# Performance work log

Hardware: AMD Instinct MI355X
Metric: run time of the kernel (lower is better)

Reference implementation:

```python
import jax, jax.numpy as jnp
import numpy as np

N_NODES = 50000
N_EDGES = 1600000
HIDDEN = 128
SPATIAL = 3
SCORE_HIDDEN = 128
EPS = 1e-12


def setup_inputs() -> dict:
    key = jax.random.key(0)
    ks = jax.random.split(key, 12)
    s = 0.02
    return {
        "h": jax.random.normal(ks[0], (N_NODES, HIDDEN), dtype=jnp.float32),
        "edge_index": jax.random.randint(ks[1], (2, N_EDGES), 0, N_NODES, dtype=jnp.int64),
        "rel_pos": jax.random.normal(ks[2], (N_EDGES, SPATIAL), dtype=jnp.float32),
        "distance": jax.random.uniform(ks[3], (N_EDGES, 1), dtype=jnp.float32),
        "node_weight": jax.random.uniform(ks[4], (N_NODES,), dtype=jnp.float32),
        "W1": jax.random.normal(ks[5], (2 * HIDDEN + SPATIAL + 1, SCORE_HIDDEN), dtype=jnp.float32) * s,
        "b1": jnp.zeros((SCORE_HIDDEN,), dtype=jnp.float32),
        "W2": jax.random.normal(ks[6], (SCORE_HIDDEN, SCORE_HIDDEN), dtype=jnp.float32) * s,
        "b2": jnp.zeros((SCORE_HIDDEN,), dtype=jnp.float32),
        "W3": jax.random.normal(ks[7], (SCORE_HIDDEN, 1), dtype=jnp.float32) * s,
        "b3": jnp.zeros((1,), dtype=jnp.float32),
        "Wv": jax.random.normal(ks[8], (HIDDEN, HIDDEN), dtype=jnp.float32) * s,
    }


def reference(h, edge_index, rel_pos, distance, node_weight, W1, b1, W2, b2, W3, b3, Wv):
    num_nodes = h.shape[0]
    dst, src = edge_index[0], edge_index[1]
    # per-edge gathered feature: [E, 2*H + spatial + 1]
    edge_feat = jnp.concatenate([h[dst], h[src], rel_pos, distance], axis=-1)
    # 3-layer score MLP -> scalar score per edge
    x = jax.nn.silu(edge_feat @ W1 + b1)
    x = jax.nn.silu(x @ W2 + b2)
    scores = (x @ W3 + b3)[:, 0]  # [E]
    # edge softmax over incoming edges of each dst node
    mx = jax.ops.segment_max(scores, dst, num_segments=num_nodes)  # -inf for empty segments
    exp_scores = jnp.exp(scores - mx[dst])
    den = jax.ops.segment_sum(exp_scores, dst, num_segments=num_nodes)
    alpha = exp_scores / (den[dst] + EPS)
    # value projection, weighted message, scatter-add aggregation
    msg = (h[src] @ Wv) * (alpha * node_weight[src])[:, None]
    out = jax.ops.segment_sum(msg, dst, num_segments=num_nodes)
    return h + out
```

## Files before the change

### kernel.cpp

```cpp
#include <hip/hip_runtime.h>
#include <hip/hip_bf16.h>
#include <cstdint>
#include <cstddef>

#define N_NODES 50000
#define N_EDGES 1600000
#define HID 128
#define PCAT_N 384
#define EPSV 1e-12f

typedef __bf16 bf16_t;
typedef __bf16 bf16x8 __attribute__((ext_vector_type(8)));
typedef float f32x4 __attribute__((ext_vector_type(4)));

__device__ __forceinline__ float bf2f_lo(unsigned u) {
    return __builtin_bit_cast(float, u << 16);
}
__device__ __forceinline__ float bf2f_hi(unsigned u) {
    return __builtin_bit_cast(float, u & 0xFFFF0000u);
}
__device__ __forceinline__ unsigned short f2bf_rne(float x) {
    unsigned u = __builtin_bit_cast(unsigned, x);
    u += 0x7FFFu + ((u >> 16) & 1u);
    return (unsigned short)(u >> 16);
}
__device__ __forceinline__ float silu_f(float x) {
    return x * __builtin_amdgcn_rcpf(1.0f + __expf(-x));
}

__global__ void k_prepw(const float* __restrict__ W1, const float* __restrict__ W2,
                        const float* __restrict__ Wv, bf16_t* __restrict__ wcatT,
                        bf16_t* __restrict__ w2t) {
    int idx = blockIdx.x * blockDim.x + threadIdx.x;
    if (idx < 384 * 128) {
        int n = idx >> 7, k = idx & 127;
        float v;
        if (n < 128)      v = W1[k * 128 + n];
        else if (n < 256) v = W1[(128 + k) * 128 + (n - 128)];
        else              v = Wv[k * 128 + (n - 256)];
        wcatT[idx] = __builtin_bit_cast(bf16_t, f2bf_rne(v));
    } else if (idx < 384 * 128 + 128 * 128) {
        int j = idx - 384 * 128;
        int n = j >> 7, k = j & 127;
        w2t[j] = __builtin_bit_cast(bf16_t, f2bf_rne(W2[k * 128 + n]));
    }
}

__global__ __launch_bounds__(256) void k_nodeproj(
    const float* __restrict__ h, const bf16_t* __restrict__ wcatT,
    const float* __restrict__ nw, bf16_t* __restrict__ pcat) {
    __shared__ bf16_t As[64 * 136];
    int t = threadIdx.x;
    int r0 = blockIdx.x * 64;
    {
        int r = t >> 2, cbase = (t & 3) * 32;
        int gr = r0 + r;
        if (gr >= N_NODES) gr = 0;
        const float* src = h + (size_t)gr * 128 + cbase;
        bf16_t* dst = As + r * 136 + cbase;
#pragma unroll
        for (int i = 0; i < 4; ++i) {
            float4 v0 = *reinterpret_cast<const float4*>(src + i * 8);
            float4 v1 = *reinterpret_cast<const float4*>(src + i * 8 + 4);
            uint4 pk;
            pk.x = (unsigned)f2bf_rne(v0.x) | ((unsigned)f2bf_rne(v0.y) << 16);
            pk.y = (unsigned)f2bf_rne(v0.z) | ((unsigned)f2bf_rne(v0.w) << 16);
            pk.z = (unsigned)f2bf_rne(v1.x) | ((unsigned)f2bf_rne(v1.y) << 16);
            pk.w = (unsigned)f2bf_rne(v1.z) | ((unsigned)f2bf_rne(v1.w) << 16);
            *reinterpret_cast<uint4*>(dst + i * 8) = pk;
        }
    }
    __syncthreads();
    int lane = t & 63, w = t >> 6;
    f32x4 acc[4][6] = {};
#pragma unroll
    for (int kk = 0; kk < 4; ++kk) {
        bf16x8 af[4], bfr[6];
#pragma unroll
        for (int fm = 0; fm < 4; ++fm)
            af[fm] = *reinterpret_cast<const bf16x8*>(
                As + (fm * 16 + (lane & 15)) * 136 + kk * 32 + (lane >> 4) * 8);
#pragma unroll
        for (int fn = 0; fn < 6; ++fn) {
            int n = w * 96 + fn * 16 + (lane & 15);
            bfr[fn] = *reinterpret_cast<const bf16x8*>(
                wcatT + (size_t)n * 128 + kk * 32 + (lane >> 4) * 8);
        }
#pragma unroll
        for (int fm = 0; fm < 4; ++fm)
#pragma unroll
            for (int fn = 0; fn < 6; ++fn)
                acc[fm][fn] = __builtin_amdgcn_mfma_f32_16x16x32_bf16(
                    af[fm], bfr[fn], acc[fm][fn], 0, 0, 0);
    }
#pragma unroll
    for (int fm = 0; fm < 4; ++fm) {
#pragma unroll
        for (int j = 0; j < 4; ++j) {
            int row = r0 + fm * 16 + (lane >> 4) * 4 + j;
            if (row < N_NODES) {
                float nwv = (w >= 2) ? nw[row] : 1.0f;
#pragma unroll
                for (int fn = 0; fn < 6; ++fn) {
                    int colbase = w * 96 + fn * 16;
                    float v = acc[fm][fn][j];
                    if (colbase >= 256) v *= nwv;
                    pcat[(size_t)row * PCAT_N + colbase + (lane & 15)] =
                        __builtin_bit_cast(bf16_t, f2bf_rne(v));
                }
            }
        }
    }
}

__global__ void k_hist(const int* __restrict__ eidx, int* __restrict__ hist) {
    int stride = gridDim.x * blockDim.x;
    for (int e = blockIdx.x * blockDim.x + threadIdx.x; e < N_EDGES; e += stride)
        atomicAdd(&hist[eidx[e]], 1);
}

__global__ __launch_bounds__(1024) void k_scan(const int* __restrict__ hist,
                                               int* __restrict__ row_start,
                                               int* __restrict__ cursor) {
    __shared__ int partial[1024];
    int t = threadIdx.x;
    const int C = (N_NODES + 1023) / 1024;
    int base = t * C;
    int sum = 0;
    for (int i = 0; i < C; ++i) {
        int j = base + i;
        if (j < N_NODES) sum += hist[j];
    }
    partial[t] = sum;
    __syncthreads();
    for (int off = 1; off < 1024; off <<= 1) {
        int v = (t >= off) ? partial[t - off] : 0;
        __syncthreads();
        partial[t] += v;
        __syncthreads();
    }
    int run = partial[t] - sum;
    for (int i = 0; i < C; ++i) {
        int j = base + i;
        if (j < N_NODES) {
            row_start[j] = run;
            cursor[j] = run;
            run += hist[j];
        }
    }
    if (t == 1023) row_start[N_NODES] = partial[1023];
}

__global__ __launch_bounds__(256, 3) void k_edge(
    const bf16_t* __restrict__ pcat, const bf16_t* __restrict__ w2t,
    const int* __restrict__ eidx, const float* __restrict__ rel_pos,
    const float* __restrict__ dist, const float* __restrict__ W1,
    const float* __restrict__ b1, const float* __restrict__ b2,
    const float* __restrict__ W3, const float* __restrict__ b3,
    int* __restrict__ cursor, float* __restrict__ scores_csr,
    int* __restrict__ src_csr) {
    __shared__ bf16_t Ax[128 * 136];
    __shared__ int s_dst[128];
    __shared__ int s_src[128];
    __shared__ float4 s_rp[128];
    __shared__ float s_sc[128];

    int t = threadIdx.x;
    int e0 = blockIdx.x * 128;
    if (t < 128) {
        int e = e0 + t;
        s_dst[t] = eidx[e];
        s_src[t] = eidx[N_EDGES + e];
        s_rp[t] = make_float4(rel_pos[(size_t)e * 3], rel_pos[(size_t)e * 3 + 1],
                              rel_pos[(size_t)e * 3 + 2], dist[e]);
        s_sc[t] = b3[0];
    }
    int lane = t & 63, w = t >> 6;
    int c0 = 2 * lane;
    float wA0 = W1[256 * 128 + c0], wA1 = W1[257 * 128 + c0];
    float wA2 = W1[258 * 128 + c0], wA3 = W1[259 * 128 + c0];
    float bA = b1[c0];
    float wB0 = W1[256 * 128 + c0 + 1], wB1 = W1[257 * 128 + c0 + 1];
    float wB2 = W1[258 * 128 + c0 + 1], wB3 = W1[259 * 128 + c0 + 1];
    float bB = b1[c0 + 1];
    __syncthreads();

#pragma unroll 4
    for (int i = 0; i < 32; ++i) {
        int e = w * 32 + i;
        int dn = s_dst[e], sn = s_src[e];
        float4 rp = s_rp[e];
        unsigned pa = *reinterpret_cast<const unsigned*>(pcat + (size_t)dn * PCAT_N + c0);
        unsigned pb = *reinterpret_cast<const unsigned*>(pcat + (size_t)sn * PCAT_N + 128 + c0);
        float x0 = bf2f_lo(pa) + bf2f_lo(pb) +
                   rp.x * wA0 + rp.y * wA1 + rp.z * wA2 + rp.w * wA3 + bA;
        float x1 = bf2f_hi(pa) + bf2f_hi(pb) +
                   rp.x * wB0 + rp.y * wB1 + rp.z * wB2 + rp.w * wB3 + bB;
        float y0 = silu_f(x0), y1 = silu_f(x1);
        unsigned pk = (unsigned)f2bf_rne(y0) | ((unsigned)f2bf_rne(y1) << 16);
        *reinterpret_cast<unsigned*>(Ax + e * 136 + c0) = pk;
    }
    __syncthreads();

    int wm = w >> 1, wn = w & 1;
    f32x4 acc[4][4] = {};
#pragma unroll
    for (int kk = 0; kk < 4; ++kk) {
        bf16x8 af[4], bfr[4];
#pragma unroll
        for (int fn = 0; fn < 4; ++fn) {
            int n = wn * 64 + fn * 16 + (lane & 15);
            bfr[fn] = *reinterpret_cast<const bf16x8*>(
                w2t + (size_t)n * 128 + kk * 32 + (lane >> 4) * 8);
        }
#pragma unroll
        for (int fm = 0; fm < 4; ++fm)
            af[fm] = *reinterpret_cast<const bf16x8*>(
                Ax + (wm * 64 + fm * 16 + (lane & 15)) * 136 + kk * 32 + (lane >> 4) * 8);
#pragma unroll
        for (int fm = 0; fm < 4; ++fm)
#pragma unroll
            for (int fn = 0; fn < 4; ++fn)
                acc[fm][fn] = __builtin_amdgcn_mfma_f32_16x16x32_bf16(
                    af[fm], bfr[fn], acc[fm][fn], 0, 0, 0);
    }

    float w3v[4], b2v[4];
#pragma unroll
    for (int fn = 0; fn < 4; ++fn) {
        int n = wn * 64 + fn * 16 + (lane & 15);
        w3v[fn] = W3[n];
        b2v[fn] = b2[n];
    }
#pragma unroll
    for (int fm = 0; fm < 4; ++fm) {
        float pj[4] = {0.f, 0.f, 0.f, 0.f};
#pragma unroll
        for (int fn = 0; fn < 4; ++fn) {
#pragma unroll
            for (int j = 0; j < 4; ++j)
                pj[j] += silu_f(acc[fm][fn][j] + b2v[fn]) * w3v[fn];
        }
#pragma unroll
        for (int j = 0; j < 4; ++j) {
            float v = pj[j];
            v += __shfl_xor(v, 1);
            v += __shfl_xor(v, 2);
            v += __shfl_xor(v, 4);
            v += __shfl_xor(v, 8);
            if ((lane & 15) == 0)
                atomicAdd(&s_sc[wm * 64 + fm * 16 + (lane >> 4) * 4 + j], v);
        }
    }
    __syncthreads();
    if (t < 128) {
        int pos = atomicAdd(&cursor[s_dst[t]], 1);
        scores_csr[pos] = s_sc[t];
        src_csr[pos] = s_src[t];
    }
}

__global__ __launch_bounds__(256) void k_agg(
    const float* __restrict__ h, const bf16_t* __restrict__ pcat,
    const float* __restrict__ scores_csr, const int* __restrict__ src_csr,
    const int* __restrict__ row_start, float* __restrict__ out) {
    __shared__ float s_coef[4][64];
    __shared__ int s_sv[4][64];
    int t = threadIdx.x, lane = t & 63, w = t >> 6;
    int node = blockIdx.x * 4 + w;
    if (node >= N_NODES) return;
    int s = row_start[node];
    int deg = row_start[node + 1] - s;
    float acc0 = 0.f, acc1 = 0.f;
    if (deg > 0) {
        float mx = -1e30f;
        for (int i = lane; i < deg; i += 64)
            mx = fmaxf(mx, scores_csr[s + i]);
#pragma unroll
        for (int m = 32; m >= 1; m >>= 1) mx = fmaxf(mx, __shfl_xor(mx, m));
        float sm = 0.f;
        for (int i = lane; i < deg; i += 64)
            sm += __expf(scores_csr[s + i] - mx);
#pragma unroll
        for (int m = 32; m >= 1; m >>= 1) sm += __shfl_xor(sm, m);
        float inv = 1.0f / (sm + EPSV);
        for (int base = 0; base < deg; base += 64) {
            int i = base + lane;
            if (i < deg) {
                s_coef[w][lane] = __expf(scores_csr[s + i] - mx) * inv;
                s_sv[w][lane] = src_csr[s + i];
            }
            asm volatile("s_waitcnt lgkmcnt(0)" ::: "memory");
            int m = deg - base;
            if (m > 64) m = 64;
#pragma unroll 4
            for (int j = 0; j < m; ++j) {
                float c = s_coef[w][j];
                int sv = s_sv[w][j];
                unsigned hv = *reinterpret_cast<const unsigned*>(
                    pcat + (size_t)sv * PCAT_N + 256 + 2 * lane);
                acc0 += c * bf2f_lo(hv);
                acc1 += c * bf2f_hi(hv);
            }
            asm volatile("s_waitcnt lgkmcnt(0)" ::: "memory");
        }
    }
    size_t o = (size_t)node * 128 + 2 * lane;
    float2 hv2 = *reinterpret_cast<const float2*>(h + o);
    float2 res;
    res.x = hv2.x + acc0;
    res.y = hv2.y + acc1;
    *reinterpret_cast<float2*>(out + o) = res;
}

extern "C" void kernel_launch(void* const* d_in, const int* in_sizes, int n_in,
                              void* d_out, int out_size, void* d_ws, size_t ws_size,
                              hipStream_t stream) {
    const float* h       = (const float*)d_in[0];
    const int*   eidx    = (const int*)d_in[1];
    const float* rel_pos = (const float*)d_in[2];
    const float* dist    = (const float*)d_in[3];
    const float* nw      = (const float*)d_in[4];
    const float* W1      = (const float*)d_in[5];
    const float* b1      = (const float*)d_in[6];
    const float* W2      = (const float*)d_in[7];
    const float* b2      = (const float*)d_in[8];
    const float* W3      = (const float*)d_in[9];
    const float* b3      = (const float*)d_in[10];
    const float* Wv      = (const float*)d_in[11];
    float* out = (float*)d_out;

    char* p = (char*)d_ws;
    auto carve = [&](size_t bytes) {
        char* r = p;
        p += (bytes + 255) & ~(size_t)255;
        return r;
    };
    bf16_t* pcat      = (bf16_t*)carve((size_t)N_NODES * PCAT_N * 2);
    bf16_t* wcatT     = (bf16_t*)carve(384 * 128 * 2);
    bf16_t* w2t       = (bf16_t*)carve(128 * 128 * 2);
    float* scores_csr = (float*)carve((size_t)N_EDGES * 4);
    int* src_csr      = (int*)carve((size_t)N_EDGES * 4);
    int* hist         = (int*)carve((size_t)N_NODES * 4);
    int* row_start    = (int*)carve((size_t)(N_NODES + 1) * 4);
    int* cursor       = (int*)carve((size_t)N_NODES * 4);

    hipMemsetAsync(hist, 0, (size_t)N_NODES * 4, stream);
    k_prepw<<<256, 256, 0, stream>>>(W1, W2, Wv, wcatT, w2t);
    k_nodeproj<<<(N_NODES + 63) / 64, 256, 0, stream>>>(h, wcatT, nw, pcat);
    k_hist<<<2048, 256, 0, stream>>>(eidx, hist);
    k_scan<<<1, 1024, 0, stream>>>(hist, row_start, cursor);
    k_edge<<<N_EDGES / 128, 256, 0, stream>>>(pcat, w2t, eidx, rel_pos, dist,
                                              W1, b1, b2, W3, b3,
                                              cursor, scores_csr, src_csr);
    k_agg<<<(N_NODES + 3) / 4, 256, 0, stream>>>(h, pcat, scores_csr, src_csr,
                                                 row_start, out);
}
```

Baseline: 656.4 us.

## Process edges in dst-sorted order and fuse softmax denominator into edge kernel

Adds a scatter pass that builds a dst-sorted edge permutation, so the edge kernel processes edges in CSR order and writes exp(score) and src contiguously instead of scattering with atomics. Each block segment-reduces exp scores by dst and atomically adds them into a per-node denominator, and the aggregation kernel drops its max and sum passes. The max subtraction is removed, which risks overflow if scores grow large. Edge tiles shrink to 64 with higher occupancy bounds, and the gathers through perm are indirect.

Result: slower. 770.4 us (+17.4%).

```diff
diff --git a/kernel.cpp b/kernel.cpp
--- a/kernel.cpp
+++ b/kernel.cpp
@@ -121,7 +121,8 @@
 
 __global__ __launch_bounds__(1024) void k_scan(const int* __restrict__ hist,
                                                int* __restrict__ row_start,
-                                               int* __restrict__ cursor) {
+                                               int* __restrict__ cursor,
+                                               float* __restrict__ den) {
     __shared__ int partial[1024];
     int t = threadIdx.x;
     const int C = (N_NODES + 1023) / 1024;
@@ -145,30 +146,41 @@
         if (j < N_NODES) {
             row_start[j] = run;
             cursor[j] = run;
+            den[j] = 0.0f;
             run += hist[j];
         }
     }
     if (t == 1023) row_start[N_NODES] = partial[1023];
 }
 
-__global__ __launch_bounds__(256, 3) void k_edge(
+__global__ void k_scatter(const int* __restrict__ eidx, int* __restrict__ cursor,
+                          int* __restrict__ perm) {
+    int stride = gridDim.x * blockDim.x;
+    for (int e = blockIdx.x * blockDim.x + threadIdx.x; e < N_EDGES; e += stride) {
+        int d = eidx[e];
+        int pos = atomicAdd(&cursor[d], 1);
+        perm[pos] = e;
+    }
+}
+
+__global__ __launch_bounds__(256, 6) void k_edge(
     const bf16_t* __restrict__ pcat, const bf16_t* __restrict__ w2t,
-    const int* __restrict__ eidx, const float* __restrict__ rel_pos,
-    const float* __restrict__ dist, const float* __restrict__ W1,
-    const float* __restrict__ b1, const float* __restrict__ b2,
-    const float* __restrict__ W3, const float* __restrict__ b3,
-    int* __restrict__ cursor, float* __restrict__ scores_csr,
-    int* __restrict__ src_csr) {
-    __shared__ bf16_t Ax[128 * 136];
-    __shared__ int s_dst[128];
-    __shared__ int s_src[128];
-    __shared__ float4 s_rp[128];
-    __shared__ float s_sc[128];
+    const int* __restrict__ perm, const int* __restrict__ eidx,
+    const float* __restrict__ rel_pos, const float* __restrict__ dist,
+    const float* __restrict__ W1, const float* __restrict__ b1,
+    const float* __restrict__ b2, const float* __restrict__ W3,
+    const float* __restrict__ b3, float* __restrict__ escore,
+    int* __restrict__ src_csr, float* __restrict__ den) {
+    __shared__ bf16_t Ax[64 * 136];
+    __shared__ int s_dst[64];
+    __shared__ int s_src[64];
+    __shared__ float4 s_rp[64];
+    __shared__ float s_sc[64];
 
     int t = threadIdx.x;
-    int e0 = blockIdx.x * 128;
-    if (t < 128) {
-        int e = e0 + t;
+    int e0 = blockIdx.x * 64;
+    if (t < 64) {
+        int e = perm[e0 + t];
         s_dst[t] = eidx[e];
         s_src[t] = eidx[N_EDGES + e];
         s_rp[t] = make_float4(rel_pos[(size_t)e * 3], rel_pos[(size_t)e * 3 + 1],
@@ -186,8 +198,8 @@
     __syncthreads();
 
 #pragma unroll 4
-    for (int i = 0; i < 32; ++i) {
-        int e = w * 32 + i;
+    for (int i = 0; i < 16; ++i) {
+        int e = w * 16 + i;
         int dn = s_dst[e], sn = s_src[e];
         float4 rp = s_rp[e];
         unsigned pa = *reinterpret_cast<const unsigned*>(pcat + (size_t)dn * PCAT_N + c0);
@@ -202,33 +214,32 @@
     }
     __syncthreads();
 
-    int wm = w >> 1, wn = w & 1;
-    f32x4 acc[4][4] = {};
+    f32x4 acc[4][2] = {};
 #pragma unroll
     for (int kk = 0; kk < 4; ++kk) {
-        bf16x8 af[4], bfr[4];
-#pragma unroll
-        for (int fn = 0; fn < 4; ++fn) {
-            int n = wn * 64 + fn * 16 + (lane & 15);
+        bf16x8 af[4], bfr[2];
+#pragma unroll
+        for (int fn = 0; fn < 2; ++fn) {
+            int n = w * 32 + fn * 16 + (lane & 15);
             bfr[fn] = *reinterpret_cast<const bf16x8*>(
                 w2t + (size_t)n * 128 + kk * 32 + (lane >> 4) * 8);
         }
 #pragma unroll
         for (int fm = 0; fm < 4; ++fm)
             af[fm] = *reinterpret_cast<const bf16x8*>(
-                Ax + (wm * 64 + fm * 16 + (lane & 15)) * 136 + kk * 32 + (lane >> 4) * 8);
+                Ax + (fm * 16 + (lane & 15)) * 136 + kk * 32 + (lane >> 4) * 8);
 #pragma unroll
         for (int fm = 0; fm < 4; ++fm)
 #pragma unroll
-            for (int fn = 0; fn < 4; ++fn)
+            for (int fn = 0; fn < 2; ++fn)
                 acc[fm][fn] = __builtin_amdgcn_mfma_f32_16x16x32_bf16(
                     af[fm], bfr[fn], acc[fm][fn], 0, 0, 0);
     }
 
-    float w3v[4], b2v[4];
-#pragma unroll
-    for (int fn = 0; fn < 4; ++fn) {
-        int n = wn * 64 + fn * 16 + (lane & 15);
+    float w3v[2], b2v[2];
+#pragma unroll
+    for (int fn = 0; fn < 2; ++fn) {
+        int n = w * 32 + fn * 16 + (lane & 15);
         w3v[fn] = W3[n];
         b2v[fn] = b2[n];
     }
@@ -236,7 +247,7 @@
     for (int fm = 0; fm < 4; ++fm) {
         float pj[4] = {0.f, 0.f, 0.f, 0.f};
 #pragma unroll
-        for (int fn = 0; fn < 4; ++fn) {
+        for (int fn = 0; fn < 2; ++fn) {
 #pragma unroll
             for (int j = 0; j < 4; ++j)
                 pj[j] += silu_f(acc[fm][fn][j] + b2v[fn]) * w3v[fn];
@@ -249,21 +260,33 @@
             v += __shfl_xor(v, 4);
             v += __shfl_xor(v, 8);
             if ((lane & 15) == 0)
-                atomicAdd(&s_sc[wm * 64 + fm * 16 + (lane >> 4) * 4 + j], v);
-        }
-    }
-    __syncthreads();
-    if (t < 128) {
-        int pos = atomicAdd(&cursor[s_dst[t]], 1);
-        scores_csr[pos] = s_sc[t];
-        src_csr[pos] = s_src[t];
+                atomicAdd(&s_sc[fm * 16 + (lane >> 4) * 4 + j], v);
+        }
+    }
+    __syncthreads();
+
+    if (t < 64) {
+        float esc = __expf(s_sc[t]);
+        escore[e0 + t] = esc;
+        src_csr[e0 + t] = s_src[t];
+        int d = s_dst[t];
+        float v = esc;
+#pragma unroll
+        for (int off = 1; off <= 32; off <<= 1) {
+            float ov = __shfl_up(v, (unsigned)off);
+            int od = __shfl_up(d, (unsigned)off);
+            if (t >= off && od == d) v += ov;
+        }
+        bool end = (t == 63) || (s_dst[t + 1] != d);
+        if (end) atomicAdd(&den[d], v);
     }
 }
 
 __global__ __launch_bounds__(256) void k_agg(
     const float* __restrict__ h, const bf16_t* __restrict__ pcat,
-    const float* __restrict__ scores_csr, const int* __restrict__ src_csr,
-    const int* __restrict__ row_start, float* __restrict__ out) {
+    const float* __restrict__ escore, const int* __restrict__ src_csr,
+    const int* __restrict__ row_start, const float* __restrict__ den,
+    float* __restrict__ out) {
     __shared__ float s_coef[4][64];
     __shared__ int s_sv[4][64];
     int t = threadIdx.x, lane = t & 63, w = t >> 6;
@@ -273,21 +296,11 @@
     int deg = row_start[node + 1] - s;
     float acc0 = 0.f, acc1 = 0.f;
     if (deg > 0) {
-        float mx = -1e30f;
-        for (int i = lane; i < deg; i += 64)
-            mx = fmaxf(mx, scores_csr[s + i]);
-#pragma unroll
-        for (int m = 32; m >= 1; m >>= 1) mx = fmaxf(mx, __shfl_xor(mx, m));
-        float sm = 0.f;
-        for (int i = lane; i < deg; i += 64)
-            sm += __expf(scores_csr[s + i] - mx);
-#pragma unroll
-        for (int m = 32; m >= 1; m >>= 1) sm += __shfl_xor(sm, m);
-        float inv = 1.0f / (sm + EPSV);
+        float inv = __builtin_amdgcn_rcpf(den[node] + EPSV);
         for (int base = 0; base < deg; base += 64) {
             int i = base + lane;
             if (i < deg) {
-                s_coef[w][lane] = __expf(scores_csr[s + i] - mx) * inv;
+                s_coef[w][lane] = escore[s + i] * inv;
                 s_sv[w][lane] = src_csr[s + i];
             }
             asm volatile("s_waitcnt lgkmcnt(0)" ::: "memory");
@@ -336,23 +349,26 @@
         p += (bytes + 255) & ~(size_t)255;
         return r;
     };
-    bf16_t* pcat      = (bf16_t*)carve((size_t)N_NODES * PCAT_N * 2);
-    bf16_t* wcatT     = (bf16_t*)carve(384 * 128 * 2);
-    bf16_t* w2t       = (bf16_t*)carve(128 * 128 * 2);
-    float* scores_csr = (float*)carve((size_t)N_EDGES * 4);
-    int* src_csr      = (int*)carve((size_t)N_EDGES * 4);
-    int* hist         = (int*)carve((size_t)N_NODES * 4);
-    int* row_start    = (int*)carve((size_t)(N_NODES + 1) * 4);
-    int* cursor       = (int*)carve((size_t)N_NODES * 4);
+    bf16_t* pcat    = (bf16_t*)carve((size_t)N_NODES * PCAT_N * 2);
+    bf16_t* wcatT   = (bf16_t*)carve(384 * 128 * 2);
+    bf16_t* w2t     = (bf16_t*)carve(128 * 128 * 2);
+    float* escore   = (float*)carve((size_t)N_EDGES * 4);
+    int* src_csr    = (int*)carve((size_t)N_EDGES * 4);
+    int* perm       = (int*)carve((size_t)N_EDGES * 4);
+    int* hist       = (int*)carve((size_t)N_NODES * 4);
+    int* row_start  = (int*)carve((size_t)(N_NODES + 1) * 4);
+    int* cursor     = (int*)carve((size_t)N_NODES * 4);
+    float* den      = (float*)carve((size_t)N_NODES * 4);
 
     hipMemsetAsync(hist, 0, (size_t)N_NODES * 4, stream);
     k_prepw<<<256, 256, 0, stream>>>(W1, W2, Wv, wcatT, w2t);
     k_nodeproj<<<(N_NODES + 63) / 64, 256, 0, stream>>>(h, wcatT, nw, pcat);
     k_hist<<<2048, 256, 0, stream>>>(eidx, hist);
-    k_scan<<<1, 1024, 0, stream>>>(hist, row_start, cursor);
-    k_edge<<<N_EDGES / 128, 256, 0, stream>>>(pcat, w2t, eidx, rel_pos, dist,
-                                              W1, b1, b2, W3, b3,
-                                              cursor, scores_csr, src_csr);
-    k_agg<<<(N_NODES + 3) / 4, 256, 0, stream>>>(h, pcat, scores_csr, src_csr,
-                                                 row_start, out);
-}
+    k_scan<<<1, 1024, 0, stream>>>(hist, row_start, cursor, den);
+    k_scatter<<<2048, 256, 0, stream>>>(eidx, cursor, perm);
+    k_edge<<<N_EDGES / 64, 256, 0, stream>>>(pcat, w2t, perm, eidx, rel_pos,
+                                             dist, W1, b1, b2, W3, b3,
+                                             escore, src_csr, den);
+    k_agg<<<(N_NODES + 3) / 4, 256, 0, stream>>>(h, pcat, escore, src_csr,
+                                                 row_start, den, out);
+}
```
